# Optimization experiments

Hardware: AMD Instinct MI355X
Metric: run time of the kernel (lower is better)

The kernel has to match this reference:

```python
import jax, jax.numpy as jnp
import numpy as np

B, N, K, S_IN, S_OUT, C, FD = 32, 325, 20, 12, 12, 10, 64
ALPHA = 0.5  # LeakyReLU negative slope

def leaky(x):
    return jnp.where(x >= 0, x, ALPHA * x)

def setup_inputs() -> dict:
    key = jax.random.key(0)
    ks = jax.random.split(key, 9)
    s = 0.2
    return {
        "fushed_features": jax.random.normal(ks[0], (B, N, FD), jnp.float32),
        "input_data": jax.random.normal(ks[1], (B, N, S_IN), jnp.float32),
        "w_W": jax.random.normal(ks[2], (S_IN, S_OUT), jnp.float32) * s,
        "w_b": jax.random.normal(ks[3], (S_OUT,), jnp.float32) * s,
        "a1_W": jax.random.normal(ks[4], (2 * S_OUT, 4 * S_OUT), jnp.float32) * s,
        "a1_b": jax.random.normal(ks[5], (4 * S_OUT,), jnp.float32) * s,
        "a2_W": jax.random.normal(ks[6], (4 * S_OUT, C), jnp.float32) * s,
        "a2_b": jax.random.normal(ks[7], (C,), jnp.float32) * s,
        "adj_mx_topk_index": jax.random.randint(ks[8], (B, N, K), 0, N),
    }

def reference(fushed_features, input_data, w_W, w_b, a1_W, a1_b, a2_W, a2_b, adj_mx_topk_index):
    # w_net: Linear + LeakyReLU -> wh [B,N,S_OUT]
    wh = leaky(input_data @ w_W + w_b)
    # a_net on cat([wh_i, wh_j]): split first linear to avoid materializing [B,N,N,2*S_OUT]
    hx = wh @ a1_W[:S_OUT]   # contribution of wh_x (row node i)
    hy = wh @ a1_W[S_OUT:]   # contribution of wh_y (col node j)
    hidden = leaky(hx[:, :, None, :] + hy[:, None, :, :] + a1_b)   # [B,N,N,4*S_OUT]
    attention = leaky(hidden @ a2_W + a2_b)                        # [B,N,N,C]
    idx = adj_mx_topk_index                                        # [B,N,K]
    # gather top-k neighbors along dim 2
    idx_c = jnp.broadcast_to(idx[..., None], idx.shape + (attention.shape[-1],))
    attention_mask = jnp.take_along_axis(attention, idx_c, axis=2)  # [B,N,K,C]
    attention_mask = jax.nn.softmax(attention_mask, axis=-1)
    # gather neighbor features: wh_expand_top_k[b,i,k] = wh[b, idx[b,i,k]]
    wh_topk = wh[jnp.arange(wh.shape[0])[:, None, None], idx]       # [B,N,K,S_OUT]
    # output = attention_mask^T @ wh_topk
    output_data = jnp.einsum('bnkc,bnks->bncs', attention_mask, wh_topk)
    # clustering loss on detached neighbor features (cosine similarity)
    wt = jax.lax.stop_gradient(wh_topk)
    wtn = wt / (jnp.linalg.norm(wt, axis=-1, keepdims=True) + 1e-8)
    dist_mat = jnp.einsum('bnks,bnls->bnkl', wtn, wtn)              # [B,N,K,K]
    same = (dist_mat >= 0.5).astype(dist_mat.dtype)
    diff = 1.0 - same
    prob = jnp.einsum('bnkc,bnlc->bnkl', attention_mask, attention_mask)
    prob = jnp.clip(prob, 1e-4, 1.0 - 1e-4)
    logp = jnp.log(prob)
    cl = -(same * logp - diff * logp)
    cluster_loss = (cl.sum((-1, -2)) - jnp.trace(cl, axis1=-2, axis2=-1)).mean()
    return output_data, cluster_loss, dist_mat.mean(), wh.mean()
```

## Files before the change

kernel.cpp:

```cpp
#include <hip/hip_runtime.h>
#include <math.h>

#define Bdim 32
#define Ndim 325
#define Kdim 20
#define Sdim 12
#define Cdim 10
#define Hdim 48
#define NB   (Bdim*Ndim)
#define OUT_SCALARS (NB*Cdim*Sdim)
#define Tpairs (Kdim*(Kdim-1)/2)
#define BN_BLOCKS (NB/4)
#define NODE_BLOCKS 260
#define NPB 40

#define O_WH  0
#define O_HX  (O_WH + NB*Sdim)
#define O_HY  (O_HX + NB*Hdim)
#define O_PCL (O_HY + NB*Hdim)
#define O_PDS (O_PCL + BN_BLOCKS)
#define O_PWH (O_PDS + BN_BLOCKS)
#define O_ATT (O_PWH + NODE_BLOCKS)
#define WS_BASE_FLOATS (O_ATT + NB*Kdim*12)

__device__ __forceinline__ float leaky(float x) { return x >= 0.f ? x : 0.5f * x; }

__global__ __launch_bounds__(256)
void node_kernel(const float* __restrict__ x,
                 const float* __restrict__ wW, const float* __restrict__ wb,
                 const float* __restrict__ A1, const float* __restrict__ b1,
                 float* __restrict__ ws)
{
    __shared__ float s_wh[NPB][Sdim];
    __shared__ float s_r[4];
    const int tid = threadIdx.x;
    const int base = blockIdx.x * NPB;

    float v = 0.f;
    #pragma unroll
    for (int rep = 0; rep < 2; rep++) {
        const int e = tid + rep * 256;
        if (e < NPB * Sdim) {
            const int n = e / Sdim, s = e - n * Sdim;
            const float* xr = x + (size_t)(base + n) * Sdim;
            float acc = wb[s];
            #pragma unroll
            for (int i = 0; i < Sdim; i++) acc += xr[i] * wW[i * Sdim + s];
            acc = leaky(acc);
            s_wh[n][s] = acc;
            ws[O_WH + (size_t)(base + n) * Sdim + s] = acc;
            v += acc;
        }
    }
    __syncthreads();

    #pragma unroll
    for (int rep = 0; rep < 15; rep++) {
        const int e = tid + rep * 256;
        const int n = e / 96, r = e - n * 96;
        const int which = r / Hdim, d = r - which * Hdim;
        const float4 w0 = *(const float4*)&s_wh[n][0];
        const float4 w1 = *(const float4*)&s_wh[n][4];
        const float4 w2 = *(const float4*)&s_wh[n][8];
        const float* Ac = A1 + (which * Sdim) * Hdim + d;
        float acc = which ? 0.f : b1[d];
        acc += w0.x*Ac[0*Hdim] + w0.y*Ac[1*Hdim] + w0.z*Ac[2*Hdim] + w0.w*Ac[3*Hdim]
             + w1.x*Ac[4*Hdim] + w1.y*Ac[5*Hdim] + w1.z*Ac[6*Hdim] + w1.w*Ac[7*Hdim]
             + w2.x*Ac[8*Hdim] + w2.y*Ac[9*Hdim] + w2.z*Ac[10*Hdim] + w2.w*Ac[11*Hdim];
        ws[(which ? O_HY : O_HX) + (size_t)(base + n) * Hdim + d] = acc;
    }

    #pragma unroll
    for (int off = 32; off > 0; off >>= 1) v += __shfl_down(v, off);
    if ((tid & 63) == 0) s_r[tid >> 6] = v;
    __syncthreads();
    if (tid == 0) ws[O_PWH + blockIdx.x] = s_r[0] + s_r[1] + s_r[2] + s_r[3];
}

__global__ __launch_bounds__(256)
void att_kernel(const int* __restrict__ topk,
                const float* __restrict__ A2, const float* __restrict__ b2,
                float* __restrict__ ws)
{
    const int gid = blockIdx.x * 256 + threadIdx.x;
    if (gid >= NB * Kdim) return;
    const int bn = gid / Kdim;
    const int b  = bn / Ndim;
    const int j  = topk[gid];

    const float4* hx4 = (const float4*)(ws + O_HX + (size_t)bn * Hdim);
    const float4* hy4 = (const float4*)(ws + O_HY + ((size_t)b * Ndim + j) * Hdim);

    float acc[Cdim];
    #pragma unroll
    for (int c = 0; c < Cdim; c++) acc[c] = b2[c];
    #pragma unroll
    for (int q = 0; q < 12; q++) {
        const float4 xv = hx4[q], yv = hy4[q];
        const float hh[4] = { leaky(xv.x + yv.x), leaky(xv.y + yv.y),
                              leaky(xv.z + yv.z), leaky(xv.w + yv.w) };
        #pragma unroll
        for (int i = 0; i < 4; i++) {
            #pragma unroll
            for (int c = 0; c < Cdim; c++)
                acc[c] += hh[i] * A2[(q * 4 + i) * Cdim + c];
        }
    }
    float m = -1e30f;
    #pragma unroll
    for (int c = 0; c < Cdim; c++) { acc[c] = leaky(acc[c]); m = fmaxf(m, acc[c]); }
    float sum = 0.f;
    #pragma unroll
    for (int c = 0; c < Cdim; c++) { acc[c] = __expf(acc[c] - m); sum += acc[c]; }
    const float inv = 1.f / sum;

    float* ar = ws + O_ATT + (size_t)gid * 12;
    *(float4*)(ar + 0) = make_float4(acc[0]*inv, acc[1]*inv, acc[2]*inv, acc[3]*inv);
    *(float4*)(ar + 4) = make_float4(acc[4]*inv, acc[5]*inv, acc[6]*inv, acc[7]*inv);
    *(float4*)(ar + 8) = make_float4(acc[8]*inv, acc[9]*inv, 0.f, 0.f);
}

__global__ __launch_bounds__(256)
void bn_kernel(const int* __restrict__ topk,
               float* __restrict__ ws, float* __restrict__ out)
{
    __shared__ float s_whj [4][Kdim][12];
    __shared__ float s_am  [4][Kdim][12];
    __shared__ float s_invn[4][Kdim];
    __shared__ int   s_idx [4][Kdim];
    __shared__ float s_red[2][4];

    const int tid = threadIdx.x;
    const int slot = tid >> 6, t = tid & 63;
    const int bn = blockIdx.x * 4 + slot, b = bn / Ndim;

    if (t < Kdim) s_idx[slot][t] = topk[(size_t)bn * Kdim + t];
    __builtin_amdgcn_wave_barrier();

    if (t < 60) {
        const int k = t / 3, q = t - k * 3;
        const float4 v = *(const float4*)(ws + O_WH + ((size_t)b * Ndim + s_idx[slot][k]) * Sdim + q * 4);
        *(float4*)&s_whj[slot][k][q * 4] = v;
        const float4 a = *(const float4*)(ws + O_ATT + (size_t)bn * (Kdim * 12) + t * 4);
        *(float4*)&s_am[slot][k][q * 4] = a;
    }
    __builtin_amdgcn_wave_barrier();

    float cl = 0.f, ds = 0.f;

    if (t < Kdim) {
        const float4 w0 = *(const float4*)&s_whj[slot][t][0];
        const float4 w1 = *(const float4*)&s_whj[slot][t][4];
        const float4 w2 = *(const float4*)&s_whj[slot][t][8];
        const float nn = w0.x*w0.x + w0.y*w0.y + w0.z*w0.z + w0.w*w0.w
                       + w1.x*w1.x + w1.y*w1.y + w1.z*w1.z + w1.w*w1.w
                       + w2.x*w2.x + w2.y*w2.y + w2.z*w2.z + w2.w*w2.w;
        const float invn = 1.f / (sqrtf(nn) + 1e-8f);
        s_invn[slot][t] = invn;
        ds += nn * invn * invn;
    } else if (t < Kdim + 30) {
        const int e = t - Kdim, c = e / 3, sq = e - c * 3;
        float4 o = make_float4(0.f, 0.f, 0.f, 0.f);
        #pragma unroll
        for (int k = 0; k < Kdim; k++) {
            const float a = s_am[slot][k][c];
            const float4 w = *(const float4*)&s_whj[slot][k][sq * 4];
            o.x += a * w.x; o.y += a * w.y; o.z += a * w.z; o.w += a * w.w;
        }
        *(float4*)(out + (size_t)bn * (Cdim * Sdim) + c * Sdim + sq * 4) = o;
    }
    __builtin_amdgcn_wave_barrier();

    #pragma unroll
    for (int it = 0; it < 3; it++) {
        const int e = t + it * 64;
        if (e < Tpairs) {
            const int r = Tpairs - 1 - e;
            const int m = (int)((sqrtf((float)(8 * r + 1)) - 1.f) * 0.5f + 1e-4f);
            const int k = Kdim - 2 - m;
            const int l = Kdim - 1 - (r - (m * (m + 1)) / 2);

            const float4 a0 = *(const float4*)&s_whj[slot][k][0];
            const float4 a1 = *(const float4*)&s_whj[slot][k][4];
            const float4 a2 = *(const float4*)&s_whj[slot][k][8];
            const float4 c0 = *(const float4*)&s_whj[slot][l][0];
            const float4 c1 = *(const float4*)&s_whj[slot][l][4];
            const float4 c2 = *(const float4*)&s_whj[slot][l][8];
            const float draw = a0.x*c0.x + a0.y*c0.y + a0.z*c0.z + a0.w*c0.w
                             + a1.x*c1.x + a1.y*c1.y + a1.z*c1.z + a1.w*c1.w
                             + a2.x*c2.x + a2.y*c2.y + a2.z*c2.z + a2.w*c2.w;
            const float d = draw * s_invn[slot][k] * s_invn[slot][l];

            const float4 p0 = *(const float4*)&s_am[slot][k][0];
            const float4 p1 = *(const float4*)&s_am[slot][k][4];
            const float4 p2 = *(const float4*)&s_am[slot][k][8];
            const float4 q0 = *(const float4*)&s_am[slot][l][0];
            const float4 q1 = *(const float4*)&s_am[slot][l][4];
            const float4 q2 = *(const float4*)&s_am[slot][l][8];
            float p = p0.x*q0.x + p0.y*q0.y + p0.z*q0.z + p0.w*q0.w
                    + p1.x*q1.x + p1.y*q1.y + p1.z*q1.z + p1.w*q1.w
                    + p2.x*q2.x + p2.y*q2.y + p2.z*q2.z + p2.w*q2.w;

            p = fminf(fmaxf(p, 1e-4f), 1.f - 1e-4f);
            const float lp = __logf(p);
            ds += 2.f * d;
            cl += 2.f * ((d >= 0.5f) ? -lp : lp);
        }
    }

    #pragma unroll
    for (int off = 32; off > 0; off >>= 1) {
        cl += __shfl_down(cl, off);
        ds += __shfl_down(ds, off);
    }
    if (t == 0) { s_red[0][slot] = cl; s_red[1][slot] = ds; }
    __syncthreads();
    if (tid == 0) {
        ws[O_PCL + blockIdx.x] = s_red[0][0] + s_red[0][1] + s_red[0][2] + s_red[0][3];
        ws[O_PDS + blockIdx.x] = s_red[1][0] + s_red[1][1] + s_red[1][2] + s_red[1][3];
    }
}

__global__ __launch_bounds__(1024)
void finalize(const float* __restrict__ ws, float* __restrict__ out)
{
    const int t = threadIdx.x;
    float cl = 0.f, ds = 0.f, wm = 0.f;
    for (int i = t; i < BN_BLOCKS; i += 1024) {
        cl += ws[O_PCL + i]; ds += ws[O_PDS + i];
    }
    if (t < NODE_BLOCKS) wm = ws[O_PWH + t];
    #pragma unroll
    for (int off = 32; off > 0; off >>= 1) {
        cl += __shfl_down(cl, off);
        ds += __shfl_down(ds, off);
        wm += __shfl_down(wm, off);
    }
    __shared__ float r[3][16];
    const int w = t >> 6, lane = t & 63;
    if (lane == 0) { r[0][w] = cl; r[1][w] = ds; r[2][w] = wm; }
    __syncthreads();
    if (t == 0) {
        float c = 0.f, d = 0.f, m = 0.f;
        #pragma unroll
        for (int i = 0; i < 16; i++) { c += r[0][i]; d += r[1][i]; m += r[2][i]; }
        out[OUT_SCALARS + 0] = c * (1.f / (float)NB);
        out[OUT_SCALARS + 1] = d * (1.f / ((float)NB * Kdim * Kdim));
        out[OUT_SCALARS + 2] = m * (1.f / ((float)NB * Sdim));
    }
}

__global__ void zero_scalars(float* out) {
    const int t = threadIdx.x;
    if (t < 3) out[OUT_SCALARS + t] = 0.f;
}

__global__ __launch_bounds__(64)
void fused_kernel(const float* __restrict__ input_data,
                  const float* __restrict__ w_W,  const float* __restrict__ w_b,
                  const float* __restrict__ a1_W, const float* __restrict__ a1_b,
                  const float* __restrict__ a2_W, const float* __restrict__ a2_b,
                  const int*   __restrict__ topk,
                  float* __restrict__ out)
{
    __shared__ float s_wW[Sdim * Sdim];
    __shared__ float s_wb[Sdim];
    __shared__ float s_A1[2 * Sdim * Hdim];
    __shared__ float s_b1[Hdim];
    __shared__ float s_A2f[Hdim * Cdim];
    __shared__ float s_b2f[Cdim];
    __shared__ float s_whs[Sdim];
    __shared__ float s_hx[Hdim];
    __shared__ float s_whj[Kdim][Sdim + 1];
    __shared__ float s_hid[Kdim][Hdim + 1];
    __shared__ float s_am [Kdim][Cdim + 1];
    __shared__ float s_wtn[Kdim][Sdim + 1];
    __shared__ int   s_idx[Kdim];

    const int t = threadIdx.x, bn = blockIdx.x, b = bn / Ndim;

    for (int i = t; i < Sdim * Sdim; i += 64)      s_wW[i] = w_W[i];
    if (t < Sdim)                                  s_wb[t] = w_b[t];
    for (int i = t; i < 2 * Sdim * Hdim; i += 64)  s_A1[i] = a1_W[i];
    if (t < Hdim)                                  s_b1[t] = a1_b[t];
    for (int i = t; i < Hdim * Cdim; i += 64)      s_A2f[i] = a2_W[i];
    if (t < Cdim)                                  s_b2f[t] = a2_b[t];
    if (t < Kdim)                                  s_idx[t] = topk[(size_t)bn * Kdim + t];
    __syncthreads();

    const float* xs = input_data + (size_t)bn * Sdim;
    if (t < Sdim) {
        float acc = s_wb[t];
        #pragma unroll
        for (int i = 0; i < Sdim; i++) acc += xs[i] * s_wW[i * Sdim + t];
        s_whs[t] = leaky(acc);
    }
    __syncthreads();

    if (t < Hdim) {
        float acc = 0.f;
        #pragma unroll
        for (int s = 0; s < Sdim; s++) acc += s_whs[s] * s_A1[s * Hdim + t];
        s_hx[t] = acc;
    }
    for (int e = t; e < Kdim * Sdim; e += 64) {
        const int k = e / Sdim, ss = e - k * Sdim;
        const float* xj = input_data + ((size_t)b * Ndim + s_idx[k]) * Sdim;
        float acc = s_wb[ss];
        #pragma unroll
        for (int i = 0; i < Sdim; i++) acc += xj[i] * s_wW[i * Sdim + ss];
        s_whj[k][ss] = leaky(acc);
    }
    __syncthreads();

    for (int e = t; e < Kdim * Hdim; e += 64) {
        const int k = e / Hdim, d = e - k * Hdim;
        float acc = s_hx[d] + s_b1[d];
        #pragma unroll
        for (int s = 0; s < Sdim; s++) acc += s_whj[k][s] * s_A1[(Sdim + s) * Hdim + d];
        s_hid[k][d] = leaky(acc);
    }
    __syncthreads();

    for (int e = t; e < Kdim * Cdim; e += 64) {
        const int k = e / Cdim, c = e - k * Cdim;
        float acc = s_b2f[c];
        #pragma unroll
        for (int d = 0; d < Hdim; d++) acc += s_hid[k][d] * s_A2f[d * Cdim + c];
        s_am[k][c] = leaky(acc);
    }
    __syncthreads();

    if (t < Kdim) {
        float m = -1e30f;
        #pragma unroll
        for (int c = 0; c < Cdim; c++) m = fmaxf(m, s_am[t][c]);
        float ex[Cdim]; float sum = 0.f;
        #pragma unroll
        for (int c = 0; c < Cdim; c++) { ex[c] = expf(s_am[t][c] - m); sum += ex[c]; }
        const float inv = 1.f / sum;
        #pragma unroll
        for (int c = 0; c < Cdim; c++) s_am[t][c] = ex[c] * inv;
        float nn = 0.f;
        #pragma unroll
        for (int s = 0; s < Sdim; s++) nn += s_whj[t][s] * s_whj[t][s];
        const float invn = 1.f / (sqrtf(nn) + 1e-8f);
        #pragma unroll
        for (int s = 0; s < Sdim; s++) s_wtn[t][s] = s_whj[t][s] * invn;
    }
    __syncthreads();

    float* op = out + (size_t)bn * (Cdim * Sdim);
    for (int e = t; e < Cdim * Sdim; e += 64) {
        const int c = e / Sdim, ss = e - c * Sdim;
        float acc = 0.f;
        #pragma unroll
        for (int k = 0; k < Kdim; k++) acc += s_am[k][c] * s_whj[k][ss];
        op[e] = acc;
    }

    float cl = 0.f, ds = 0.f;
    for (int e = t; e < Kdim * Kdim; e += 64) {
        const int k = e / Kdim, l = e - k * Kdim;
        float d = 0.f;
        #pragma unroll
        for (int s = 0; s < Sdim; s++) d += s_wtn[k][s] * s_wtn[l][s];
        ds += d;
        if (k != l) {
            float p = 0.f;
            #pragma unroll
            for (int c = 0; c < Cdim; c++) p += s_am[k][c] * s_am[l][c];
            p = fminf(fmaxf(p, 1e-4f), 1.f - 1e-4f);
            const float lp = logf(p);
            cl += (d >= 0.5f) ? -lp : lp;
        }
    }
    float whl = (t < Sdim) ? s_whs[t] : 0.f;
    #pragma unroll
    for (int off = 32; off > 0; off >>= 1) {
        cl  += __shfl_down(cl,  off);
        ds  += __shfl_down(ds,  off);
        whl += __shfl_down(whl, off);
    }
    if (t == 0) {
        atomicAdd(&out[OUT_SCALARS + 0], cl  * (1.f / (float)NB));
        atomicAdd(&out[OUT_SCALARS + 1], ds  * (1.f / ((float)NB * Kdim * Kdim)));
        atomicAdd(&out[OUT_SCALARS + 2], whl * (1.f / ((float)NB * Sdim)));
    }
}

extern "C" void kernel_launch(void* const* d_in, const int* in_sizes, int n_in,
                              void* d_out, int out_size, void* d_ws, size_t ws_size,
                              hipStream_t stream) {
    (void)in_sizes; (void)n_in; (void)out_size;
    const float* input_data = (const float*)d_in[1];
    const float* w_W  = (const float*)d_in[2];
    const float* w_b  = (const float*)d_in[3];
    const float* a1_W = (const float*)d_in[4];
    const float* a1_b = (const float*)d_in[5];
    const float* a2_W = (const float*)d_in[6];
    const float* a2_b = (const float*)d_in[7];
    const int*   topk = (const int*)d_in[8];
    float* out = (float*)d_out;
    float* ws  = (float*)d_ws;

    if (ws_size >= (size_t)WS_BASE_FLOATS * sizeof(float)) {
        hipLaunchKernelGGL(node_kernel, dim3(NODE_BLOCKS), dim3(256), 0, stream,
                           input_data, w_W, w_b, a1_W, a1_b, ws);
        hipLaunchKernelGGL(att_kernel, dim3((NB * Kdim + 255) / 256), dim3(256), 0, stream,
                           topk, a2_W, a2_b, ws);
        hipLaunchKernelGGL(bn_kernel, dim3(BN_BLOCKS), dim3(256), 0, stream,
                           topk, ws, out);
        hipLaunchKernelGGL(finalize, dim3(1), dim3(1024), 0, stream, ws, out);
    } else {
        hipLaunchKernelGGL(zero_scalars, dim3(1), dim3(64), 0, stream, out);
        hipLaunchKernelGGL(fused_kernel, dim3(NB), dim3(64), 0, stream,
                           input_data, w_W, w_b, a1_W, a1_b, a2_W, a2_b, topk, out);
    }
}
```

Measured before the change: 109.8 us.

## Fuse attention computation into per-node kernel, dropping attention workspace round-trip

Merges the attention-softmax kernel into the per-node cluster/output kernel: 80 threads of each block compute the 80 (node, neighbor) softmax rows straight into shared memory while the remaining threads gather neighbor features. This removes one launch and the global write/read of the padded attention buffer. The trade-off is that only 80 of 256 threads do the heavy MLP work per block, and a full block barrier replaces the per-wave barriers, so the per-block compute becomes less balanced.

```diff
diff --git a/kernel.cpp b/kernel.cpp
--- a/kernel.cpp
+++ b/kernel.cpp
@@ -20,8 +20,7 @@
 #define O_PCL (O_HY + NB*Hdim)
 #define O_PDS (O_PCL + BN_BLOCKS)
 #define O_PWH (O_PDS + BN_BLOCKS)
-#define O_ATT (O_PWH + NODE_BLOCKS)
-#define WS_BASE_FLOATS (O_ATT + NB*Kdim*12)
+#define WS_BASE_FLOATS (O_PWH + NODE_BLOCKS)
 
 __device__ __forceinline__ float leaky(float x) { return x >= 0.f ? x : 0.5f * x; }
 
@@ -78,74 +77,68 @@
 }
 
 __global__ __launch_bounds__(256)
-void att_kernel(const int* __restrict__ topk,
-                const float* __restrict__ A2, const float* __restrict__ b2,
-                float* __restrict__ ws)
-{
-    const int gid = blockIdx.x * 256 + threadIdx.x;
-    if (gid >= NB * Kdim) return;
-    const int bn = gid / Kdim;
-    const int b  = bn / Ndim;
-    const int j  = topk[gid];
-
-    const float4* hx4 = (const float4*)(ws + O_HX + (size_t)bn * Hdim);
-    const float4* hy4 = (const float4*)(ws + O_HY + ((size_t)b * Ndim + j) * Hdim);
-
-    float acc[Cdim];
-    #pragma unroll
-    for (int c = 0; c < Cdim; c++) acc[c] = b2[c];
-    #pragma unroll
-    for (int q = 0; q < 12; q++) {
-        const float4 xv = hx4[q], yv = hy4[q];
-        const float hh[4] = { leaky(xv.x + yv.x), leaky(xv.y + yv.y),
-                              leaky(xv.z + yv.z), leaky(xv.w + yv.w) };
-        #pragma unroll
-        for (int i = 0; i < 4; i++) {
-            #pragma unroll
-            for (int c = 0; c < Cdim; c++)
-                acc[c] += hh[i] * A2[(q * 4 + i) * Cdim + c];
-        }
-    }
-    float m = -1e30f;
-    #pragma unroll
-    for (int c = 0; c < Cdim; c++) { acc[c] = leaky(acc[c]); m = fmaxf(m, acc[c]); }
-    float sum = 0.f;
-    #pragma unroll
-    for (int c = 0; c < Cdim; c++) { acc[c] = __expf(acc[c] - m); sum += acc[c]; }
-    const float inv = 1.f / sum;
-
-    float* ar = ws + O_ATT + (size_t)gid * 12;
-    *(float4*)(ar + 0) = make_float4(acc[0]*inv, acc[1]*inv, acc[2]*inv, acc[3]*inv);
-    *(float4*)(ar + 4) = make_float4(acc[4]*inv, acc[5]*inv, acc[6]*inv, acc[7]*inv);
-    *(float4*)(ar + 8) = make_float4(acc[8]*inv, acc[9]*inv, 0.f, 0.f);
-}
-
-__global__ __launch_bounds__(256)
-void bn_kernel(const int* __restrict__ topk,
-               float* __restrict__ ws, float* __restrict__ out)
+void mega_kernel(const int* __restrict__ topk,
+                 const float* __restrict__ A2, const float* __restrict__ b2,
+                 float* __restrict__ ws, float* __restrict__ out)
 {
     __shared__ float s_whj [4][Kdim][12];
     __shared__ float s_am  [4][Kdim][12];
     __shared__ float s_invn[4][Kdim];
-    __shared__ int   s_idx [4][Kdim];
     __shared__ float s_red[2][4];
 
     const int tid = threadIdx.x;
     const int slot = tid >> 6, t = tid & 63;
-    const int bn = blockIdx.x * 4 + slot, b = bn / Ndim;
-
-    if (t < Kdim) s_idx[slot][t] = topk[(size_t)bn * Kdim + t];
-    __builtin_amdgcn_wave_barrier();
-
-    if (t < 60) {
-        const int k = t / 3, q = t - k * 3;
-        const float4 v = *(const float4*)(ws + O_WH + ((size_t)b * Ndim + s_idx[slot][k]) * Sdim + q * 4);
-        *(float4*)&s_whj[slot][k][q * 4] = v;
-        const float4 a = *(const float4*)(ws + O_ATT + (size_t)bn * (Kdim * 12) + t * 4);
-        *(float4*)&s_am[slot][k][q * 4] = a;
-    }
-    __builtin_amdgcn_wave_barrier();
-
+
+    if (tid < 80) {
+        const int gid = blockIdx.x * 80 + tid;
+        const int bn_e = gid / Kdim;
+        const int b_e  = bn_e / Ndim;
+        const int j    = topk[gid];
+        const int ek   = tid / 20, kk = tid - ek * 20;
+
+        const float4* hx4 = (const float4*)(ws + O_HX + (size_t)bn_e * Hdim);
+        const float4* hy4 = (const float4*)(ws + O_HY + ((size_t)b_e * Ndim + j) * Hdim);
+
+        float acc[Cdim];
+        #pragma unroll
+        for (int c = 0; c < Cdim; c++) acc[c] = b2[c];
+        #pragma unroll
+        for (int q = 0; q < 12; q++) {
+            const float4 xv = hx4[q], yv = hy4[q];
+            const float hh[4] = { leaky(xv.x + yv.x), leaky(xv.y + yv.y),
+                                  leaky(xv.z + yv.z), leaky(xv.w + yv.w) };
+            #pragma unroll
+            for (int i = 0; i < 4; i++) {
+                #pragma unroll
+                for (int c = 0; c < Cdim; c++)
+                    acc[c] += hh[i] * A2[(q * 4 + i) * Cdim + c];
+            }
+        }
+        float m = -1e30f;
+        #pragma unroll
+        for (int c = 0; c < Cdim; c++) { acc[c] = leaky(acc[c]); m = fmaxf(m, acc[c]); }
+        float sum = 0.f;
+        #pragma unroll
+        for (int c = 0; c < Cdim; c++) { acc[c] = __expf(acc[c] - m); sum += acc[c]; }
+        const float inv = 1.f / sum;
+        *(float4*)&s_am[ek][kk][0] = make_float4(acc[0]*inv, acc[1]*inv, acc[2]*inv, acc[3]*inv);
+        *(float4*)&s_am[ek][kk][4] = make_float4(acc[4]*inv, acc[5]*inv, acc[6]*inv, acc[7]*inv);
+        *(float4*)&s_am[ek][kk][8] = make_float4(acc[8]*inv, acc[9]*inv, 0.f, 0.f);
+    } else {
+        for (int i = tid - 80; i < 240; i += 176) {
+            const int kf = i / 3, q = i - kf * 3;
+            const int sl = kf / 20, k = kf - sl * 20;
+            const int gidx = blockIdx.x * 80 + kf;
+            const int bn_i = gidx / Kdim;
+            const int b_i  = bn_i / Ndim;
+            const int j    = topk[gidx];
+            const float4 v = *(const float4*)(ws + O_WH + ((size_t)b_i * Ndim + j) * Sdim + q * 4);
+            *(float4*)&s_whj[sl][k][q * 4] = v;
+        }
+    }
+    __syncthreads();
+
+    const int bn = blockIdx.x * 4 + slot;
     float cl = 0.f, ds = 0.f;
 
     if (t < Kdim) {
@@ -407,10 +400,8 @@
     if (ws_size >= (size_t)WS_BASE_FLOATS * sizeof(float)) {
         hipLaunchKernelGGL(node_kernel, dim3(NODE_BLOCKS), dim3(256), 0, stream,
                            input_data, w_W, w_b, a1_W, a1_b, ws);
-        hipLaunchKernelGGL(att_kernel, dim3((NB * Kdim + 255) / 256), dim3(256), 0, stream,
-                           topk, a2_W, a2_b, ws);
-        hipLaunchKernelGGL(bn_kernel, dim3(BN_BLOCKS), dim3(256), 0, stream,
-                           topk, ws, out);
+        hipLaunchKernelGGL(mega_kernel, dim3(BN_BLOCKS), dim3(256), 0, stream,
+                           topk, a2_W, a2_b, ws, out);
         hipLaunchKernelGGL(finalize, dim3(1), dim3(1024), 0, stream, ws, out);
     } else {
         hipLaunchKernelGGL(zero_scalars, dim3(1), dim3(64), 0, stream, out);
```

After: 106.2 us. 1.03x faster.
